# Kernel tuning notes

Hardware: AMD Instinct MI355X
Metric: run time of the kernel (lower is better)

## Reference

```python
import jax, jax.numpy as jnp
import numpy as np

# db4 decomposition low-pass filter (pywt convention, 8 taps)
DEC_LO = np.array([-0.010597401784997278, 0.032883011666982945, 0.030841381835986965,
                   -0.18703481171888114, -0.02798376941698385, 0.6308807679295904,
                   0.7148465705525415, 0.23037781330885523], dtype=np.float32)
L = DEC_LO.shape[0]  # 8
REC_LO = DEC_LO[::-1].copy()
DEC_HI = (REC_LO * ((-1.0) ** (np.arange(L) + 1))).astype(np.float32)
REC_HI = DEC_HI[::-1].copy()
LEVEL = 7

# lax.conv does correlation; flip filters to get true convolution (pywt semantics)
K_DEC = jnp.asarray(np.stack([DEC_LO[::-1], DEC_HI[::-1]])[:, None, :])  # [2,1,L] out-ch: (lo, hi)
K_REC = jnp.asarray(np.stack([REC_LO[::-1], REC_HI[::-1]])[None, :, :])  # [1,2,L] in-ch: (ca, cd)


def dwt(x):
    # x: [B, N]. pywt zero-mode dwt == full conv then take odd indices;
    # fused here as stride-2 conv with asymmetric padding (L-2, L-1).
    y = jax.lax.conv_general_dilated(x[:, None, :], K_DEC, (2,), [(L - 2, L - 1)])
    return y[:, 0], y[:, 1]  # each [B, floor((N+L-1)/2)]


def idwt(ca, cd):
    # upsample-by-2 (lhs_dilation, length 2n-1), full conv, trim L-2 each side -> pad (1,1)
    y = jax.lax.conv_general_dilated(jnp.stack([ca, cd], axis=1), K_REC, (1,),
                                     [(1, 1)], lhs_dilation=(2,))
    return y[:, 0]  # [B, 2n - L + 2]


def soft(c, t):
    # pywt.threshold(mode='soft')
    return jnp.sign(c) * jnp.maximum(jnp.abs(c) - t, 0.0)


def setup_inputs() -> dict:
    key = jax.random.key(0)
    k1, k2 = jax.random.split(key)
    x = jax.random.normal(k1, (32768, 1116), dtype=jnp.float32)
    # learned scalar parameter, initialized like nn.Parameter(torch.tensor(0.02))
    raw_threshold = jnp.asarray(0.02, dtype=jnp.float32)
    return {"x": x, "raw_threshold": raw_threshold}


def reference(x, raw_threshold):
    thr = jnp.maximum(raw_threshold, 0.01)  # torch.clamp(min=0.01)
    # wavedec: 7-level analysis
    a = x
    details = []
    for _ in range(LEVEL):
        a, d = dwt(a)
        details.append(d)
    # soft-threshold every coefficient band (including approximation)
    a = soft(a, thr)
    details = [soft(d, thr) for d in details]
    # waverec: synthesis, truncating cA when one sample longer than cD (pywt rule)
    for d in reversed(details):
        if a.shape[-1] > d.shape[-1]:
            a = a[:, : d.shape[-1]]
        a = idwt(a, d)
    return a  # [B, 1116]
```

## Files before the change

kernel.cpp:

```cpp
#include <hip/hip_runtime.h>

#define NCOL 1116
#define NLEV 7
#define NT 256

static __device__ __forceinline__ float softf(float c, float t) {
    float m = fabsf(c) - t;
    return m > 0.0f ? copysignf(m, c) : 0.0f;
}

__global__ __launch_bounds__(NT)
void wavelet_kernel(const float* __restrict__ x,
                    const float* __restrict__ thr_ptr,
                    float* __restrict__ out) {
    constexpr float DEC_LO[8] = {-0.010597401784997278f,  0.032883011666982945f,
                                  0.030841381835986965f, -0.18703481171888114f,
                                 -0.02798376941698385f,   0.6308807679295904f,
                                  0.7148465705525415f,    0.23037781330885523f};
    constexpr float DEC_HI[8] = {-0.23037781330885523f,   0.7148465705525415f,
                                 -0.6308807679295904f,   -0.02798376941698385f,
                                  0.18703481171888114f,   0.030841381835986965f,
                                 -0.032883011666982945f, -0.010597401784997278f};
    constexpr float REC_LO[8] = { 0.23037781330885523f,   0.7148465705525415f,
                                  0.6308807679295904f,   -0.02798376941698385f,
                                 -0.18703481171888114f,   0.030841381835986965f,
                                  0.032883011666982945f, -0.010597401784997278f};
    constexpr float REC_HI[8] = {-0.010597401784997278f, -0.032883011666982945f,
                                  0.030841381835986965f,  0.18703481171888114f,
                                 -0.02798376941698385f,  -0.6308807679295904f,
                                  0.7148465705525415f,   -0.23037781330885523f};

    constexpr int alen[8] = {1116, 561, 284, 145, 76, 41, 24, 15};
    constexpr int doff[7] = {0, 561, 845, 990, 1066, 1107, 1131};

    __shared__ float A[1132];
    __shared__ float B[578];
    __shared__ float D[1146];

    const int tid = threadIdx.x;
    const int row = blockIdx.x;
    const float thr = fmaxf(thr_ptr[0], 0.01f);

    float* a0 = A + 8;
    float* b0 = B + 8;

    {
        const float4* xr = (const float4*)(x + (size_t)row * NCOL);
        float4* dst = (float4*)a0;
        for (int i = tid; i < NCOL / 4; i += NT) dst[i] = xr[i];
        if (tid < 8) { A[tid] = 0.0f; a0[NCOL + tid] = 0.0f; }
    }
    __syncthreads();

    float* cur = a0;
    float* nxt = b0;
    #pragma unroll
    for (int l = 0; l < NLEV; ++l) {
        const int nout = alen[l + 1];
        float* dp = D + doff[l];
        for (int o = tid; o < nout; o += NT) {
            const float* src = cur + 2 * o + 1;
            float lo = 0.0f, hi = 0.0f;
            #pragma unroll
            for (int s = 0; s < 8; ++s) {
                float v = src[-s];
                lo = fmaf(DEC_LO[s], v, lo);
                hi = fmaf(DEC_HI[s], v, hi);
            }
            nxt[o] = lo;
            dp[o] = softf(hi, thr);
        }
        if (tid < 8) { nxt[-8 + tid] = 0.0f; nxt[nout + tid] = 0.0f; }
        float* t = cur; cur = nxt; nxt = t;
        __syncthreads();
    }

    if (tid < 15) cur[tid] = softf(cur[tid], thr);
    __syncthreads();

    #pragma unroll
    for (int l = NLEV - 1; l >= 0; --l) {
        const int M = alen[l + 1];
        const float* dp = D + doff[l];
        const int npair = M - 3;
        if (l > 0) {
            for (int m = tid; m < npair; m += NT) {
                float ca0 = cur[m], ca1 = cur[m + 1], ca2 = cur[m + 2], ca3 = cur[m + 3];
                float cd0 = dp[m],  cd1 = dp[m + 1],  cd2 = dp[m + 2],  cd3 = dp[m + 3];
                float y0 = fmaf(REC_LO[0], ca3, fmaf(REC_LO[2], ca2, fmaf(REC_LO[4], ca1, REC_LO[6] * ca0)));
                y0 = fmaf(REC_HI[0], cd3, fmaf(REC_HI[2], cd2, fmaf(REC_HI[4], cd1, fmaf(REC_HI[6], cd0, y0))));
                float y1 = fmaf(REC_LO[1], ca3, fmaf(REC_LO[3], ca2, fmaf(REC_LO[5], ca1, REC_LO[7] * ca0)));
                y1 = fmaf(REC_HI[1], cd3, fmaf(REC_HI[3], cd2, fmaf(REC_HI[5], cd1, fmaf(REC_HI[7], cd0, y1))));
                nxt[2 * m] = y0;
                nxt[2 * m + 1] = y1;
            }
            float* t = cur; cur = nxt; nxt = t;
            __syncthreads();
        } else {
            float2* orow = (float2*)(out + (size_t)row * NCOL);
            for (int m = tid; m < npair; m += NT) {
                float ca0 = cur[m], ca1 = cur[m + 1], ca2 = cur[m + 2], ca3 = cur[m + 3];
                float cd0 = dp[m],  cd1 = dp[m + 1],  cd2 = dp[m + 2],  cd3 = dp[m + 3];
                float y0 = fmaf(REC_LO[0], ca3, fmaf(REC_LO[2], ca2, fmaf(REC_LO[4], ca1, REC_LO[6] * ca0)));
                y0 = fmaf(REC_HI[0], cd3, fmaf(REC_HI[2], cd2, fmaf(REC_HI[4], cd1, fmaf(REC_HI[6], cd0, y0))));
                float y1 = fmaf(REC_LO[1], ca3, fmaf(REC_LO[3], ca2, fmaf(REC_LO[5], ca1, REC_LO[7] * ca0)));
                y1 = fmaf(REC_HI[1], cd3, fmaf(REC_HI[3], cd2, fmaf(REC_HI[5], cd1, fmaf(REC_HI[7], cd0, y1))));
                orow[m] = make_float2(y0, y1);
            }
        }
    }
}

extern "C" void kernel_launch(void* const* d_in, const int* in_sizes, int n_in,
                              void* d_out, int out_size, void* d_ws, size_t ws_size,
                              hipStream_t stream) {
    const float* x = (const float*)d_in[0];
    const float* thr = (const float*)d_in[1];
    float* out = (float*)d_out;
    const int nrow = in_sizes[0] / NCOL;
    hipLaunchKernelGGL(wavelet_kernel, dim3(nrow), dim3(NT), 0, stream, x, thr, out);
}
```

Baseline: 268.5 us.

## Map one wavefront per row with private LDS arena and wave barriers

Each 64-lane wavefront now processes a whole row inside its own shared-memory arena, so four rows run per block. This replaces block-wide __syncthreads with wave-level barriers and removes idle threads on the small deeper levels. Each lane also computes two outputs per iteration, reusing overlapping loads, and writes with vector float2/float4 stores. In exchange each wave does more serial work on the large first level, and shared memory per block grows, which may limit occupancy.

```diff
diff --git a/kernel.cpp b/kernel.cpp
--- a/kernel.cpp
+++ b/kernel.cpp
@@ -3,6 +3,8 @@
 #define NCOL 1116
 #define NLEV 7
 #define NT 256
+#define RPB 4
+#define ARENA 2048
 
 static __device__ __forceinline__ float softf(float c, float t) {
     float m = fabsf(c) - t;
@@ -12,7 +14,7 @@
 __global__ __launch_bounds__(NT)
 void wavelet_kernel(const float* __restrict__ x,
                     const float* __restrict__ thr_ptr,
-                    float* __restrict__ out) {
+                    float* __restrict__ out, int nrow) {
     constexpr float DEC_LO[8] = {-0.010597401784997278f,  0.032883011666982945f,
                                   0.030841381835986965f, -0.18703481171888114f,
                                  -0.02798376941698385f,   0.6308807679295904f,
@@ -31,81 +33,123 @@
                                   0.7148465705525415f,   -0.23037781330885523f};
 
     constexpr int alen[8] = {1116, 561, 284, 145, 76, 41, 24, 15};
-    constexpr int doff[7] = {0, 561, 845, 990, 1066, 1107, 1131};
+    constexpr int doff[7] = {8, 570, 854, 1000, 1076, 2008, 2032};
 
-    __shared__ float A[1132];
-    __shared__ float B[578];
-    __shared__ float D[1146];
+    __shared__ __align__(16) float SH[RPB * ARENA];
 
-    const int tid = threadIdx.x;
-    const int row = blockIdx.x;
+    const int lane = threadIdx.x & 63;
+    const int wv   = threadIdx.x >> 6;
+    const int row  = blockIdx.x * RPB + wv;
+    if (row >= nrow) return;
+
     const float thr = fmaxf(thr_ptr[0], 0.01f);
 
-    float* a0 = A + 8;
-    float* b0 = B + 8;
+    float* const arena = SH + wv * ARENA;
+    float* const a8 = arena + 8;
+    float* const b8 = arena + 1140;
+    float* const c8 = arena + 1716;
 
     {
         const float4* xr = (const float4*)(x + (size_t)row * NCOL);
-        float4* dst = (float4*)a0;
-        for (int i = tid; i < NCOL / 4; i += NT) dst[i] = xr[i];
-        if (tid < 8) { A[tid] = 0.0f; a0[NCOL + tid] = 0.0f; }
+        float4* dst = (float4*)a8;
+        for (int i = lane; i < NCOL / 4; i += 64) dst[i] = xr[i];
+        if (lane < 14) { int j = lane < 6 ? lane - 6 : 1110 + lane; a8[j] = 0.0f; }
     }
-    __syncthreads();
+    __builtin_amdgcn_wave_barrier();
 
-    float* cur = a0;
-    float* nxt = b0;
-    #pragma unroll
-    for (int l = 0; l < NLEV; ++l) {
-        const int nout = alen[l + 1];
-        float* dp = D + doff[l];
-        for (int o = tid; o < nout; o += NT) {
-            const float* src = cur + 2 * o + 1;
-            float lo = 0.0f, hi = 0.0f;
-            #pragma unroll
-            for (int s = 0; s < 8; ++s) {
-                float v = src[-s];
-                lo = fmaf(DEC_LO[s], v, lo);
-                hi = fmaf(DEC_HI[s], v, hi);
+    {
+        float* cur = a8;
+        float* nxt = b8;
+        #pragma unroll
+        for (int l = 0; l < NLEV; ++l) {
+            const int nout = alen[l + 1];
+            float* dp = arena + doff[l];
+            for (int b = lane; 2 * b < nout; b += 64) {
+                const int o = 2 * b;
+                const float* src = cur + o + o - 6;
+                float v[10];
+                #pragma unroll
+                for (int j = 0; j < 10; ++j) v[j] = src[j];
+                float lo0 = 0.f, hi0 = 0.f, lo1 = 0.f, hi1 = 0.f;
+                #pragma unroll
+                for (int s = 0; s < 8; ++s) {
+                    lo0 = fmaf(DEC_LO[s], v[7 - s], lo0);
+                    hi0 = fmaf(DEC_HI[s], v[7 - s], hi0);
+                    lo1 = fmaf(DEC_LO[s], v[9 - s], lo1);
+                    hi1 = fmaf(DEC_HI[s], v[9 - s], hi1);
+                }
+                float av0 = (l == NLEV - 1) ? softf(lo0, thr) : lo0;
+                float dv0 = softf(hi0, thr);
+                if (o + 1 < nout) {
+                    float av1 = (l == NLEV - 1) ? softf(lo1, thr) : lo1;
+                    *(float2*)(nxt + o) = make_float2(av0, av1);
+                    *(float2*)(dp + o)  = make_float2(dv0, softf(hi1, thr));
+                } else {
+                    nxt[o] = av0;
+                    dp[o]  = dv0;
+                }
             }
-            nxt[o] = lo;
-            dp[o] = softf(hi, thr);
+            if (l < NLEV - 1) {
+                if (lane < 15) {
+                    int j = lane < 6 ? lane - 6 : nout + lane - 6;
+                    nxt[j] = 0.0f;
+                }
+            }
+            __builtin_amdgcn_wave_barrier();
+            if (l == 0) { cur = b8; nxt = c8; }
+            else       { float* t = cur; cur = nxt; nxt = t; }
         }
-        if (tid < 8) { nxt[-8 + tid] = 0.0f; nxt[nout + tid] = 0.0f; }
-        float* t = cur; cur = nxt; nxt = t;
-        __syncthreads();
     }
 
-    if (tid < 15) cur[tid] = softf(cur[tid], thr);
-    __syncthreads();
-
-    #pragma unroll
-    for (int l = NLEV - 1; l >= 0; --l) {
-        const int M = alen[l + 1];
-        const float* dp = D + doff[l];
-        const int npair = M - 3;
-        if (l > 0) {
-            for (int m = tid; m < npair; m += NT) {
-                float ca0 = cur[m], ca1 = cur[m + 1], ca2 = cur[m + 2], ca3 = cur[m + 3];
-                float cd0 = dp[m],  cd1 = dp[m + 1],  cd2 = dp[m + 2],  cd3 = dp[m + 3];
-                float y0 = fmaf(REC_LO[0], ca3, fmaf(REC_LO[2], ca2, fmaf(REC_LO[4], ca1, REC_LO[6] * ca0)));
-                y0 = fmaf(REC_HI[0], cd3, fmaf(REC_HI[2], cd2, fmaf(REC_HI[4], cd1, fmaf(REC_HI[6], cd0, y0))));
-                float y1 = fmaf(REC_LO[1], ca3, fmaf(REC_LO[3], ca2, fmaf(REC_LO[5], ca1, REC_LO[7] * ca0)));
-                y1 = fmaf(REC_HI[1], cd3, fmaf(REC_HI[3], cd2, fmaf(REC_HI[5], cd1, fmaf(REC_HI[7], cd0, y1))));
-                nxt[2 * m] = y0;
-                nxt[2 * m + 1] = y1;
+    {
+        float* cur = b8;
+        float* nxt = c8;
+        #pragma unroll
+        for (int l = NLEV - 1; l >= 1; --l) {
+            const int M = alen[l + 1];
+            const float* dp = arena + doff[l];
+            const int npair = M - 3;
+            for (int b = lane; 2 * b < npair; b += 64) {
+                const int m = 2 * b;
+                float ca[5], cd[5];
+                #pragma unroll
+                for (int j = 0; j < 5; ++j) { ca[j] = cur[m + j]; cd[j] = dp[m + j]; }
+                float y0 = fmaf(REC_LO[0], ca[3], fmaf(REC_LO[2], ca[2], fmaf(REC_LO[4], ca[1], REC_LO[6] * ca[0])));
+                y0 = fmaf(REC_HI[0], cd[3], fmaf(REC_HI[2], cd[2], fmaf(REC_HI[4], cd[1], fmaf(REC_HI[6], cd[0], y0))));
+                float y1 = fmaf(REC_LO[1], ca[3], fmaf(REC_LO[3], ca[2], fmaf(REC_LO[5], ca[1], REC_LO[7] * ca[0])));
+                y1 = fmaf(REC_HI[1], cd[3], fmaf(REC_HI[3], cd[2], fmaf(REC_HI[5], cd[1], fmaf(REC_HI[7], cd[0], y1))));
+                if (m + 1 < npair) {
+                    float y2 = fmaf(REC_LO[0], ca[4], fmaf(REC_LO[2], ca[3], fmaf(REC_LO[4], ca[2], REC_LO[6] * ca[1])));
+                    y2 = fmaf(REC_HI[0], cd[4], fmaf(REC_HI[2], cd[3], fmaf(REC_HI[4], cd[2], fmaf(REC_HI[6], cd[1], y2))));
+                    float y3 = fmaf(REC_LO[1], ca[4], fmaf(REC_LO[3], ca[3], fmaf(REC_LO[5], ca[2], REC_LO[7] * ca[1])));
+                    y3 = fmaf(REC_HI[1], cd[4], fmaf(REC_HI[3], cd[3], fmaf(REC_HI[5], cd[2], fmaf(REC_HI[7], cd[1], y3))));
+                    *(float4*)(nxt + 2 * m) = make_float4(y0, y1, y2, y3);
+                } else {
+                    nxt[2 * m]     = y0;
+                    nxt[2 * m + 1] = y1;
+                }
             }
+            __builtin_amdgcn_wave_barrier();
             float* t = cur; cur = nxt; nxt = t;
-            __syncthreads();
-        } else {
-            float2* orow = (float2*)(out + (size_t)row * NCOL);
-            for (int m = tid; m < npair; m += NT) {
-                float ca0 = cur[m], ca1 = cur[m + 1], ca2 = cur[m + 2], ca3 = cur[m + 3];
-                float cd0 = dp[m],  cd1 = dp[m + 1],  cd2 = dp[m + 2],  cd3 = dp[m + 3];
-                float y0 = fmaf(REC_LO[0], ca3, fmaf(REC_LO[2], ca2, fmaf(REC_LO[4], ca1, REC_LO[6] * ca0)));
-                y0 = fmaf(REC_HI[0], cd3, fmaf(REC_HI[2], cd2, fmaf(REC_HI[4], cd1, fmaf(REC_HI[6], cd0, y0))));
-                float y1 = fmaf(REC_LO[1], ca3, fmaf(REC_LO[3], ca2, fmaf(REC_LO[5], ca1, REC_LO[7] * ca0)));
-                y1 = fmaf(REC_HI[1], cd3, fmaf(REC_HI[3], cd2, fmaf(REC_HI[5], cd1, fmaf(REC_HI[7], cd0, y1))));
-                orow[m] = make_float2(y0, y1);
+        }
+        {
+            const float* dp = arena + doff[0];
+            float4* orow = (float4*)(out + (size_t)row * NCOL);
+            const int npair = alen[1] - 3;
+            for (int b = lane; 2 * b < npair; b += 64) {
+                const int m = 2 * b;
+                float ca[5], cd[5];
+                #pragma unroll
+                for (int j = 0; j < 5; ++j) { ca[j] = cur[m + j]; cd[j] = dp[m + j]; }
+                float y0 = fmaf(REC_LO[0], ca[3], fmaf(REC_LO[2], ca[2], fmaf(REC_LO[4], ca[1], REC_LO[6] * ca[0])));
+                y0 = fmaf(REC_HI[0], cd[3], fmaf(REC_HI[2], cd[2], fmaf(REC_HI[4], cd[1], fmaf(REC_HI[6], cd[0], y0))));
+                float y1 = fmaf(REC_LO[1], ca[3], fmaf(REC_LO[3], ca[2], fmaf(REC_LO[5], ca[1], REC_LO[7] * ca[0])));
+                y1 = fmaf(REC_HI[1], cd[3], fmaf(REC_HI[3], cd[2], fmaf(REC_HI[5], cd[1], fmaf(REC_HI[7], cd[0], y1))));
+                float y2 = fmaf(REC_LO[0], ca[4], fmaf(REC_LO[2], ca[3], fmaf(REC_LO[4], ca[2], REC_LO[6] * ca[1])));
+                y2 = fmaf(REC_HI[0], cd[4], fmaf(REC_HI[2], cd[3], fmaf(REC_HI[4], cd[2], fmaf(REC_HI[6], cd[1], y2))));
+                float y3 = fmaf(REC_LO[1], ca[4], fmaf(REC_LO[3], ca[3], fmaf(REC_LO[5], ca[2], REC_LO[7] * ca[1])));
+                y3 = fmaf(REC_HI[1], cd[4], fmaf(REC_HI[3], cd[3], fmaf(REC_HI[5], cd[2], fmaf(REC_HI[7], cd[1], y3))));
+                orow[b] = make_float4(y0, y1, y2, y3);
             }
         }
     }
@@ -118,5 +162,6 @@
     const float* thr = (const float*)d_in[1];
     float* out = (float*)d_out;
     const int nrow = in_sizes[0] / NCOL;
-    hipLaunchKernelGGL(wavelet_kernel, dim3(nrow), dim3(NT), 0, stream, x, thr, out);
+    const int nblk = (nrow + RPB - 1) / RPB;
+    hipLaunchKernelGGL(wavelet_kernel, dim3(nblk), dim3(NT), 0, stream, x, thr, out, nrow);
 }
```

After: 273.3 us. No clear change (+1.8%).
